# Kernel tuning notes

Hardware: AMD Instinct MI355X
Metric: run time of the kernel (lower is better)

The kernel has to match this reference:

```python
import jax, jax.numpy as jnp
import numpy as np

# BTT dims for in=out=4096, square mode: m=n=64, a=b=64, rank=8
M, N, A, B_BLK, RANK = 64, 64, 64, 64, 8
OUT_FEATURES = M * A  # 4096


def setup_inputs() -> dict:
    key = jax.random.key(0)
    k_x, k_r, k_l = jax.random.split(key, 3)
    x = jax.random.normal(k_x, (4, 1024, 4096), dtype=jnp.float32)
    # btt_r: (n, b, m*rank); btt_l: (m, rank*n, a)
    btt_r = jax.random.normal(k_r, (N, B_BLK, M * RANK), dtype=jnp.float32) * 0.02
    btt_l = jax.random.normal(k_l, (M, RANK * N, A), dtype=jnp.float32) * 0.02
    bias = jnp.zeros((OUT_FEATURES,), dtype=jnp.float32)
    return {"x": x, "btt_r": btt_r, "btt_l": btt_l, "bias": bias}


def reference(x, btt_r, btt_l, bias):
    n, b, mr = btt_r.shape
    m, rn, a = btt_l.shape
    rank = mr // m
    orig_shape = x.shape
    xr = x.reshape(-1, n, b)          # (B, n, b)
    Bn = xr.shape[0]
    # first contraction: bmm over n blocks -> (n, B, m*rank)
    inner = jnp.einsum('Bnb,nbj->nBj', xr, btt_r)
    # reshape/permute exactly as torch: (n,B,m,r) -> (m,B,n,r) -> (m,B,n*r)
    inner = inner.reshape(n, Bn, m, rank).transpose(2, 1, 0, 3).reshape(m, Bn, rank * n)
    # second contraction: bmm over m blocks -> (B, m, a)
    out = jnp.einsum('mBk,mka->Bma', inner, btt_l)
    out = out.reshape(*orig_shape[:-1], m * a)
    return out + bias
```

## Files before the change

### kernel.cpp

```cpp
#include <hip/hip_runtime.h>


typedef float f32x16 __attribute__((ext_vector_type(16)));
typedef short short8 __attribute__((ext_vector_type(8)));

static __device__ __forceinline__ unsigned short f2b(float f) {
    union { float f; unsigned u; } a; a.f = f;
    unsigned u = a.u;
    unsigned r = u + 0x7fffu + ((u >> 16) & 1u);
    return (unsigned short)(r >> 16);
}

static __device__ __forceinline__ void load_lds_16(const void* gptr, void* lptr) {
    __builtin_amdgcn_global_load_lds(
        (const __attribute__((address_space(1))) unsigned int*)gptr,
        (__attribute__((address_space(3))) unsigned int*)lptr, 16, 0, 0);
}

__global__ __launch_bounds__(256) void prep_all(
    const float* __restrict__ x,
    const float* __restrict__ btt_r,
    const float* __restrict__ btt_l,
    unsigned short* __restrict__ xbt,
    unsigned short* __restrict__ Wtt,
    int nx)
{
    const int tid = threadIdx.x;
    if ((int)blockIdx.x < nx) {
        unsigned i = blockIdx.x * 256 + tid;
        int row = ((i >> 12) << 3) | (i & 7);
        int g   = (i >> 3) & 511;
        float4 v0 = *(const float4*)(x + (size_t)row * 4096 + g * 8);
        float4 v1 = *(const float4*)(x + (size_t)row * 4096 + g * 8 + 4);
        unsigned short o[8];
        o[0] = f2b(v0.x); o[1] = f2b(v0.y); o[2] = f2b(v0.z); o[3] = f2b(v0.w);
        o[4] = f2b(v1.x); o[5] = f2b(v1.y); o[6] = f2b(v1.z); o[7] = f2b(v1.w);
        int it = g >> 3, q = g & 7;
        int ks = q >> 1, half = q & 1;
        int rt = row >> 7, a2 = (row >> 5) & 3, l31 = row & 31;
        size_t dst = (((size_t)(rt * 64 + it) * 16 + a2 * 4 + ks) * 64 + half * 32 + l31) * 8;
        *(uint4*)(xbt + dst) = *(const uint4*)o;
        return;
    }
    __shared__ float Rs[64][8];
    __shared__ float Ls[8][64];
    const int wb = blockIdx.x - nx;
    const int m = wb >> 6, n = wb & 63;

    if (tid < 128) {
        int b = tid >> 1, rh = (tid & 1) * 4;
        float4 v = *(const float4*)(btt_r + (size_t)n * 32768 + (size_t)b * 512 + m * 8 + rh);
        *(float4*)&Rs[b][rh] = v;
    } else {
        int t2 = (tid - 128) * 4;
        float4 v = *(const float4*)(btt_l + (size_t)m * 32768 + n * 512 + t2);
        *(float4*)&(&Ls[0][0])[t2] = v;
    }
    __syncthreads();

    const int a  = tid >> 2;
    const int bg = (tid & 3) * 16;
    float la[8];
    #pragma unroll
    for (int r = 0; r < 8; ++r) la[r] = Ls[r][a];

    unsigned short o[16];
    #pragma unroll
    for (int bb = 0; bb < 16; ++bb) {
        float acc = 0.f;
        #pragma unroll
        for (int r = 0; r < 8; ++r) acc += Rs[bg + bb][r] * la[r];
        o[bb] = f2b(acc);
    }
    int col = m * 64 + a;
    int ct = col >> 7, b2 = (col >> 5) & 3, l31 = col & 31;
    int ks = bg >> 4;
    size_t dst = (((size_t)(ct * 64 + n) * 16 + b2 * 4 + ks) * 64 + l31) * 8;
    *(uint4*)(Wtt + dst)           = *(const uint4*)&o[0];
    *(uint4*)(Wtt + dst + 32 * 8)  = *(const uint4*)&o[8];
}

__global__ __launch_bounds__(256) void gemm_btt(
    const unsigned short* __restrict__ xbt,
    const unsigned short* __restrict__ Wtt,
    const float* __restrict__ bias,
    float* __restrict__ out)
{
    __shared__ unsigned short As[16 * 512];
    __shared__ unsigned short Bs[16 * 512];

    const int tid = threadIdx.x;
    const int ct = blockIdx.x;
    const int rt = blockIdx.y;

    const int wid  = tid >> 6;
    const int l    = tid & 63;
    const int half = l >> 5;
    const int l31  = l & 31;
    const int i2base = (wid >> 1) * 2;
    const int j2base = (wid & 1) * 2;

    const unsigned short* xa = xbt + (size_t)rt * 524288;
    const unsigned short* wa = Wtt + (size_t)ct * 524288;

    f32x16 acc[2][2];
    #pragma unroll
    for (int i = 0; i < 2; ++i)
        #pragma unroll
        for (int j = 0; j < 2; ++j)
            #pragma unroll
            for (int r = 0; r < 16; ++r)
                acc[i][j][r] = 0.f;

    for (int it = 0; it < 64; ++it) {
        const size_t kb = (size_t)it * 8192;
        #pragma unroll
        for (int p = 0; p < 4; ++p) {
            int o = p * 256 + tid;
            load_lds_16(xa + kb + o * 8, &As[o * 8]);
            load_lds_16(wa + kb + o * 8, &Bs[o * 8]);
        }
        __syncthreads();

        #pragma unroll
        for (int ks = 0; ks < 4; ++ks) {
            short8 af[2], bf[2];
            #pragma unroll
            for (int i = 0; i < 2; ++i)
                af[i] = *(const short8*)&As[((i2base + i) * 4 + ks) * 512 + l * 8];
            #pragma unroll
            for (int j = 0; j < 2; ++j)
                bf[j] = *(const short8*)&Bs[((j2base + j) * 4 + ks) * 512 + l * 8];
            #pragma unroll
            for (int i = 0; i < 2; ++i)
                #pragma unroll
                for (int j = 0; j < 2; ++j)
                    acc[i][j] = __builtin_amdgcn_mfma_f32_32x32x16_bf16(
                        af[i], bf[j], acc[i][j], 0, 0, 0);
        }
        __syncthreads();
    }

    const int rowTileBase = rt * 128 + (wid >> 1) * 64;
    const int colTileBase = ct * 128 + (wid & 1) * 64;
    #pragma unroll
    for (int j = 0; j < 2; ++j) {
        const int col = colTileBase + j * 32 + l31;
        const float bv = bias[col];
        #pragma unroll
        for (int i = 0; i < 2; ++i) {
            const int rbase = rowTileBase + i * 32 + 4 * half;
            #pragma unroll
            for (int r = 0; r < 16; ++r) {
                int row = rbase + (r & 3) + 8 * (r >> 2);
                out[(size_t)row * 4096 + col] = acc[i][j][r] + bv;
            }
        }
    }
}

extern "C" void kernel_launch(void* const* d_in, const int* in_sizes, int n_in,
                              void* d_out, int out_size, void* d_ws, size_t ws_size,
                              hipStream_t stream) {
    const float* x    = (const float*)d_in[0];
    const float* r    = (const float*)d_in[1];
    const float* l    = (const float*)d_in[2];
    const float* bias = (const float*)d_in[3];
    float* out = (float*)d_out;

    unsigned short* xbt = (unsigned short*)d_ws;
    unsigned short* Wtt = (unsigned short*)d_ws + (size_t)4096 * 4096;

    const int rows = in_sizes[0] / 4096;
    const int nx = rows * 4096 / 8 / 256;

    prep_all<<<dim3(nx + 4096), dim3(256), 0, stream>>>(x, r, l, xbt, Wtt, nx);
    gemm_btt<<<dim3(32, rows / 128), dim3(256), 0, stream>>>(xbt, Wtt, bias, out);
}
```

Before: 291.5 us.

## Enlarge GEMM tile to 256x256 with multi-stage LDS pipeline and grid swizzle

Reorganizes the bf16 pre-tiled layouts into 256-row/col tiles with 16-wide k-slices. The GEMM uses 512 threads and 8 waves, each computing a 128x64 subtile, and keeps an 8-deep ring of LDS slices loaded with global_load_lds so loads run ahead of MFMA compute, with explicit vmcnt waits and one barrier per two slices. The block index is swizzled to improve L2 reuse, and MFMA issue priority is raised. The larger tile gives more reuse per load and fewer barriers, at the cost of more registers, fewer blocks (256) and tricky hand-written waitcnt logic.

```diff
diff --git a/kernel.cpp b/kernel.cpp
--- a/kernel.cpp
+++ b/kernel.cpp
@@ -35,10 +35,9 @@
         unsigned short o[8];
         o[0] = f2b(v0.x); o[1] = f2b(v0.y); o[2] = f2b(v0.z); o[3] = f2b(v0.w);
         o[4] = f2b(v1.x); o[5] = f2b(v1.y); o[6] = f2b(v1.z); o[7] = f2b(v1.w);
-        int it = g >> 3, q = g & 7;
-        int ks = q >> 1, half = q & 1;
-        int rt = row >> 7, a2 = (row >> 5) & 3, l31 = row & 31;
-        size_t dst = (((size_t)(rt * 64 + it) * 16 + a2 * 4 + ks) * 64 + half * 32 + l31) * 8;
+        int ks = g >> 1, half = g & 1;
+        int rt = row >> 8, rb = (row >> 5) & 7, l31 = row & 31;
+        size_t dst = ((((size_t)rt * 256 + ks) * 8 + rb) * 64 + half * 32 + l31) * 8;
         *(uint4*)(xbt + dst) = *(const uint4*)o;
         return;
     }
@@ -73,90 +72,130 @@
         o[bb] = f2b(acc);
     }
     int col = m * 64 + a;
-    int ct = col >> 7, b2 = (col >> 5) & 3, l31 = col & 31;
-    int ks = bg >> 4;
-    size_t dst = (((size_t)(ct * 64 + n) * 16 + b2 * 4 + ks) * 64 + l31) * 8;
+    int ct = col >> 8, rb = (col >> 5) & 7, l31 = col & 31;
+    int ks = n * 4 + (bg >> 4);
+    size_t dst = ((((size_t)ct * 256 + ks) * 8 + rb) * 64 + l31) * 8;
     *(uint4*)(Wtt + dst)           = *(const uint4*)&o[0];
     *(uint4*)(Wtt + dst + 32 * 8)  = *(const uint4*)&o[8];
 }
 
-__global__ __launch_bounds__(256) void gemm_btt(
+__global__ __launch_bounds__(512, 2) void gemm_btt(
     const unsigned short* __restrict__ xbt,
     const unsigned short* __restrict__ Wtt,
     const float* __restrict__ bias,
     float* __restrict__ out)
 {
-    __shared__ unsigned short As[16 * 512];
-    __shared__ unsigned short Bs[16 * 512];
+    __shared__ unsigned short As[8][4096];
+    __shared__ unsigned short Bs[8][4096];
 
     const int tid = threadIdx.x;
-    const int ct = blockIdx.x;
-    const int rt = blockIdx.y;
-
-    const int wid  = tid >> 6;
-    const int l    = tid & 63;
-    const int half = l >> 5;
-    const int l31  = l & 31;
-    const int i2base = (wid >> 1) * 2;
-    const int j2base = (wid & 1) * 2;
-
-    const unsigned short* xa = xbt + (size_t)rt * 524288;
-    const unsigned short* wa = Wtt + (size_t)ct * 524288;
-
-    f32x16 acc[2][2];
-    #pragma unroll
-    for (int i = 0; i < 2; ++i)
+    const int bid = blockIdx.x;
+    const int cpx = gridDim.x >> 3;
+    const int swz = (bid & 7) * cpx + (bid >> 3);
+    const int rt = swz >> 4;
+    const int ct = swz & 15;
+
+    const int wid = tid >> 6, l = tid & 63;
+    const int l31 = l & 31, half = l >> 5;
+    const int wr = wid >> 2;
+    const int wc = wid & 3;
+
+    const unsigned short* xa = xbt + (size_t)rt * (256 * 4096);
+    const unsigned short* wa = Wtt + (size_t)ct * (256 * 4096);
+
+    const int offA0 = ((wr * 4 + 0) * 64 + l) * 8;
+    const int offA1 = ((wr * 4 + 1) * 64 + l) * 8;
+    const int offA2 = ((wr * 4 + 2) * 64 + l) * 8;
+    const int offA3 = ((wr * 4 + 3) * 64 + l) * 8;
+    const int offB0 = ((wc * 2 + 0) * 64 + l) * 8;
+    const int offB1 = ((wc * 2 + 1) * 64 + l) * 8;
+
+    f32x16 acc[4][2];
+    #pragma unroll
+    for (int i = 0; i < 4; ++i)
         #pragma unroll
         for (int j = 0; j < 2; ++j)
             #pragma unroll
             for (int r = 0; r < 16; ++r)
                 acc[i][j][r] = 0.f;
 
-    for (int it = 0; it < 64; ++it) {
-        const size_t kb = (size_t)it * 8192;
-        #pragma unroll
-        for (int p = 0; p < 4; ++p) {
-            int o = p * 256 + tid;
-            load_lds_16(xa + kb + o * 8, &As[o * 8]);
-            load_lds_16(wa + kb + o * 8, &Bs[o * 8]);
-        }
-        __syncthreads();
-
-        #pragma unroll
-        for (int ks = 0; ks < 4; ++ks) {
-            short8 af[2], bf[2];
-            #pragma unroll
-            for (int i = 0; i < 2; ++i)
-                af[i] = *(const short8*)&As[((i2base + i) * 4 + ks) * 512 + l * 8];
-            #pragma unroll
-            for (int j = 0; j < 2; ++j)
-                bf[j] = *(const short8*)&Bs[((j2base + j) * 4 + ks) * 512 + l * 8];
-            #pragma unroll
-            for (int i = 0; i < 2; ++i)
-                #pragma unroll
-                for (int j = 0; j < 2; ++j)
-                    acc[i][j] = __builtin_amdgcn_mfma_f32_32x32x16_bf16(
-                        af[i], bf[j], acc[i][j], 0, 0, 0);
-        }
-        __syncthreads();
-    }
-
-    const int rowTileBase = rt * 128 + (wid >> 1) * 64;
-    const int colTileBase = ct * 128 + (wid & 1) * 64;
-    #pragma unroll
-    for (int j = 0; j < 2; ++j) {
-        const int col = colTileBase + j * 32 + l31;
+    #define STAGE(s) do {                                                    \
+        load_lds_16(xa + (size_t)(s) * 4096 + tid * 8, &As[(s) & 7][tid * 8]); \
+        load_lds_16(wa + (size_t)(s) * 4096 + tid * 8, &Bs[(s) & 7][tid * 8]); \
+    } while (0)
+
+    #define BARRIER() do {                                                   \
+        asm volatile("s_waitcnt lgkmcnt(0)" ::: "memory");                   \
+        __builtin_amdgcn_s_barrier();                                        \
+        asm volatile("" ::: "memory");                                       \
+    } while (0)
+
+    #define SLICE(s) do {                                                    \
+        const unsigned short* Ab = &As[(s) & 7][0];                          \
+        const unsigned short* Bb = &Bs[(s) & 7][0];                          \
+        short8 af0 = *(const short8*)(Ab + offA0);                           \
+        short8 af1 = *(const short8*)(Ab + offA1);                           \
+        short8 af2 = *(const short8*)(Ab + offA2);                           \
+        short8 af3 = *(const short8*)(Ab + offA3);                           \
+        short8 bf0 = *(const short8*)(Bb + offB0);                           \
+        short8 bf1 = *(const short8*)(Bb + offB1);                           \
+        __builtin_amdgcn_s_setprio(1);                                       \
+        acc[0][0] = __builtin_amdgcn_mfma_f32_32x32x16_bf16(af0, bf0, acc[0][0], 0, 0, 0); \
+        acc[0][1] = __builtin_amdgcn_mfma_f32_32x32x16_bf16(af0, bf1, acc[0][1], 0, 0, 0); \
+        acc[1][0] = __builtin_amdgcn_mfma_f32_32x32x16_bf16(af1, bf0, acc[1][0], 0, 0, 0); \
+        acc[1][1] = __builtin_amdgcn_mfma_f32_32x32x16_bf16(af1, bf1, acc[1][1], 0, 0, 0); \
+        acc[2][0] = __builtin_amdgcn_mfma_f32_32x32x16_bf16(af2, bf0, acc[2][0], 0, 0, 0); \
+        acc[2][1] = __builtin_amdgcn_mfma_f32_32x32x16_bf16(af2, bf1, acc[2][1], 0, 0, 0); \
+        acc[3][0] = __builtin_amdgcn_mfma_f32_32x32x16_bf16(af3, bf0, acc[3][0], 0, 0, 0); \
+        acc[3][1] = __builtin_amdgcn_mfma_f32_32x32x16_bf16(af3, bf1, acc[3][1], 0, 0, 0); \
+        __builtin_amdgcn_s_setprio(0);                                       \
+    } while (0)
+
+    #pragma unroll
+    for (int s = 0; s < 6; ++s) STAGE(s);
+    asm volatile("s_waitcnt vmcnt(8)" ::: "memory");
+
+    #pragma unroll 1
+    for (int j = 0; j < 125; ++j) {
+        const int s0 = 2 * j;
+        BARRIER();
+        STAGE(s0 + 6);
+        STAGE(s0 + 7);
+        asm volatile("s_waitcnt vmcnt(8)" ::: "memory");
+        SLICE(s0);
+        SLICE(s0 + 1);
+    }
+    BARRIER();
+    asm volatile("s_waitcnt vmcnt(4)" ::: "memory");
+    SLICE(250);
+    SLICE(251);
+    BARRIER();
+    asm volatile("s_waitcnt vmcnt(0)" ::: "memory");
+    SLICE(252);
+    SLICE(253);
+    BARRIER();
+    SLICE(254);
+    SLICE(255);
+
+    const int rowTileBase = rt * 256 + wr * 128;
+    const int colTileBase = ct * 256 + wc * 64;
+    #pragma unroll
+    for (int jn = 0; jn < 2; ++jn) {
+        const int col = colTileBase + jn * 32 + l31;
         const float bv = bias[col];
         #pragma unroll
-        for (int i = 0; i < 2; ++i) {
+        for (int i = 0; i < 4; ++i) {
             const int rbase = rowTileBase + i * 32 + 4 * half;
             #pragma unroll
             for (int r = 0; r < 16; ++r) {
                 int row = rbase + (r & 3) + 8 * (r >> 2);
-                out[(size_t)row * 4096 + col] = acc[i][j][r] + bv;
+                out[(size_t)row * 4096 + col] = acc[i][jn][r] + bv;
             }
         }
     }
+    #undef STAGE
+    #undef BARRIER
+    #undef SLICE
 }
 
 extern "C" void kernel_launch(void* const* d_in, const int* in_sizes, int n_in,
@@ -175,5 +214,5 @@
     const int nx = rows * 4096 / 8 / 256;
 
     prep_all<<<dim3(nx + 4096), dim3(256), 0, stream>>>(x, r, l, xbt, Wtt, nx);
-    gemm_btt<<<dim3(32, rows / 128), dim3(256), 0, stream>>>(xbt, Wtt, bias, out);
-}
+    gemm_btt<<<dim3((rows / 256) * 16), dim3(512), 0, stream>>>(xbt, Wtt, bias, out);
+}
```

Result: no change. 296.4 us (+1.7%).
